# Kernel optimization log

Hardware: AMD Instinct MI355X
Metric: run time of the kernel (lower is better)

Reference implementation:

```python
import jax, jax.numpy as jnp
import numpy as np


def bilinear_align_corners(p, H, W):
    # p: [B, C, h, w] -> [B, C, H, W], matches F.interpolate(mode='bilinear', align_corners=True)
    b, c, h, w = p.shape
    ys = jnp.linspace(0.0, h - 1.0, H)
    xs = jnp.linspace(0.0, w - 1.0, W)
    y0 = jnp.floor(ys).astype(jnp.int32)
    x0 = jnp.floor(xs).astype(jnp.int32)
    y1 = jnp.minimum(y0 + 1, h - 1)
    x1 = jnp.minimum(x0 + 1, w - 1)
    wy = (ys - y0.astype(p.dtype))[:, None]          # [H,1]
    wx = (xs - x0.astype(p.dtype))                   # [W]
    rows = p[:, :, y0, :] * (1 - wy) + p[:, :, y1, :] * wy   # [B,C,H,w]
    out = rows[:, :, :, x0] * (1 - wx) + rows[:, :, :, x1] * wx  # [B,C,H,W]
    return out


def conv1x1(x, W, b):
    return jnp.einsum('bchw,oc->bohw', x, W) + b[None, :, None, None]


def scan_axis(feat, A_bar, B_bar, axis):
    # selective recurrence h_i = A_i * stop_grad(h_{i-1}) + B_i * x_i along `axis`
    f = jnp.moveaxis(feat, axis, 0)
    A = jnp.moveaxis(A_bar, axis, 0)
    B = jnp.moveaxis(B_bar, axis, 0)

    def step(prev, inp):
        a_i, b_i, x_i = inp
        h = a_i * jax.lax.stop_gradient(prev) + b_i * x_i
        return h, h

    _, hs = jax.lax.scan(step, jnp.zeros_like(f[0]), (A, B, f))
    return jnp.moveaxis(hs, 0, axis)


def setup_inputs() -> dict:
    key = jax.random.key(0)
    ks = jax.random.split(key, 12)
    Bsz, Cin, H, W = 4, 64, 256, 256
    hid = 128
    s_in = 1.0 / np.sqrt(Cin)
    s_hid = 1.0 / np.sqrt(hid)
    return {
        'x': jax.random.normal(ks[0], (Bsz, Cin, H, W), jnp.float32),
        'prior': jax.random.normal(ks[1], (Bsz, 1, 64, 64), jnp.float32),
        'W_in': jax.random.uniform(ks[2], (hid, Cin), jnp.float32, -s_in, s_in),
        'b_in': jax.random.uniform(ks[3], (hid,), jnp.float32, -s_in, s_in),
        'W_out': jax.random.uniform(ks[4], (Cin, hid), jnp.float32, -s_hid, s_hid),
        'b_out': jax.random.uniform(ks[5], (Cin,), jnp.float32, -s_hid, s_hid),
        'W_delta': jax.random.uniform(ks[6], (hid, hid), jnp.float32, -s_hid, s_hid),
        'b_delta': jax.random.uniform(ks[7], (hid,), jnp.float32, -s_hid, s_hid),
        'W_B': jax.random.uniform(ks[8], (hid, hid), jnp.float32, -s_hid, s_hid),
        'b_B': jax.random.uniform(ks[9], (hid,), jnp.float32, -s_hid, s_hid),
        'A_param': jax.random.normal(ks[10], (hid,), jnp.float32),
        'lambda_delta': jnp.float32(0.1),
        'alpha': jnp.float32(0.1),
        'gamma': jnp.float32(0.1),
    }


def reference(x, prior, W_in, b_in, W_out, b_out, W_delta, b_delta, W_B, b_B,
              A_param, lambda_delta, alpha, gamma):
    Bsz, C, H, W = x.shape
    prior_up = jnp.clip(bilinear_align_corners(prior, H, W), -1.0, 1.0)
    x_proj = conv1x1(x, W_in, b_in)
    delta = jax.nn.softplus(conv1x1(x_proj, W_delta, b_delta) + lambda_delta * prior_up)
    B_k = conv1x1(x_proj, W_B, b_B) * (1.0 + alpha * prior_up)
    A = -jnp.exp(A_param)[None, :, None, None]
    A_bar = jnp.exp(delta * A)
    B_bar = delta * B_k
    # dim=0 in torch code scans along W (axis 3); dim=1 scans along H (axis 2)
    scanned = scan_axis(x_proj, A_bar, B_bar, 3) + scan_axis(x_proj, A_bar, B_bar, 2)
    out = conv1x1(scanned, W_out, b_out)
    return (x + gamma * out, prior_up)
```

## Files before the change

kernel.cpp:

```cpp
#include <hip/hip_runtime.h>
#include <hip/hip_bf16.h>

#define OUT1 16777216
#define BIG  33554432

typedef _Float16 half8 __attribute__((ext_vector_type(8)));
typedef float    floatx4 __attribute__((ext_vector_type(4)));

struct __align__(8) h4s { _Float16 x, y, z, w; };
__device__ inline void store4h(_Float16* p, float4 v){
    h4s t; t.x = (_Float16)v.x; t.y = (_Float16)v.y; t.z = (_Float16)v.z; t.w = (_Float16)v.w;
    *(h4s*)p = t;
}

__global__ __launch_bounds__(256) void k_prior(const float* __restrict__ prior, float* __restrict__ pu){
    int i = blockIdx.x*256 + threadIdx.x;
    int b = i >> 16;
    int rem = i & 65535;
    int yy = rem >> 8, xx = rem & 255;
    const float scale = 63.0f/255.0f;
    float sy = yy*scale, sx = xx*scale;
    int y0 = min((int)floorf(sy), 63), x0 = min((int)floorf(sx), 63);
    int y1 = min(y0+1, 63), x1 = min(x0+1, 63);
    float wy = sy - (float)y0, wx = sx - (float)x0;
    const float* pb = prior + (b<<12);
    float v00 = pb[(y0<<6)+x0], v01 = pb[(y0<<6)+x1];
    float v10 = pb[(y1<<6)+x0], v11 = pb[(y1<<6)+x1];
    float r0 = v00*(1.f-wy) + v10*wy;
    float r1 = v01*(1.f-wy) + v11*wy;
    float v  = r0*(1.f-wx) + r1*wx;
    pu[i] = fminf(fmaxf(v, -1.f), 1.f);
}

__global__ __launch_bounds__(256) void k_comb(const float* __restrict__ W_in, const float* __restrict__ b_in,
        const float* __restrict__ W_delta, const float* __restrict__ b_delta,
        const float* __restrict__ W_B, const float* __restrict__ b_B,
        const float* __restrict__ A_param, const float* __restrict__ W_out,
        _Float16* __restrict__ Wch, float* __restrict__ bcv, float* __restrict__ negA,
        _Float16* __restrict__ Wof){
    int i = blockIdx.x*256 + threadIdx.x;
    if (i < 24576){
        int r = i >> 6, c = i & 63;
        float v;
        if (r < 128) v = W_in[i];
        else if (r < 256){
            int rr = r-128; float s = 0.f;
            for (int k=0;k<128;k++) s = fmaf(W_delta[(rr<<7)+k], W_in[(k<<6)+c], s);
            v = s;
        } else {
            int rr = r-256; float s = 0.f;
            for (int k=0;k<128;k++) s = fmaf(W_B[(rr<<7)+k], W_in[(k<<6)+c], s);
            v = s;
        }
        Wch[i] = (_Float16)v;
    } else if (i < 24960){
        int r = i - 24576; float v;
        if (r < 128) v = b_in[r];
        else if (r < 256){
            int rr=r-128; float s = b_delta[rr];
            for (int k=0;k<128;k++) s = fmaf(W_delta[(rr<<7)+k], b_in[k], s);
            v = s;
        } else {
            int rr=r-256; float s = b_B[rr];
            for (int k=0;k<128;k++) s = fmaf(W_B[(rr<<7)+k], b_in[k], s);
            v = s;
        }
        bcv[r] = v;
    } else if (i < 25088){
        negA[i-24960] = -expf(A_param[i-24960]);
    } else if (i < 33280){
        Wof[i-25088] = (_Float16)W_out[i-25088];
    }
}

__global__ __launch_bounds__(512, 4) void k_proj_mfma(const float* __restrict__ x, const float* __restrict__ pu,
        const _Float16* __restrict__ Wch, const float* __restrict__ bcv, const float* __restrict__ negA,
        const float* __restrict__ lam_p, const float* __restrict__ alp_p,
        _Float16* __restrict__ Ab, _Float16* __restrict__ Uu){
    __shared__ _Float16 Ws[24576];

    const int t    = threadIdx.x;
    const int lane = t & 63;
    const int wave = t >> 6;
    const int col  = lane & 15;
    const int quad = lane >> 4;

    const int blk = blockIdx.x;
    const int b   = blk >> 9;
    const int p0  = (blk & 511) << 7;
    const int pxw = p0 + (wave << 4);

    {
        const float4* wsrc = (const float4*)Wch;
        #pragma unroll
        for (int i = 0; i < 6; i++){
            int c = t + (i << 9);
            int row = c >> 3, part = c & 7;
            float4 v = wsrc[c];
            int byteoff = ((row << 7) + (part << 4)) ^ ((row & 7) << 4);
            *(float4*)((char*)Ws + byteoff) = v;
        }
    }

    const float* xb = x + ((size_t)b<<22) + pxw + col;
    half8 aX0, aX1;
    #pragma unroll
    for (int j = 0; j < 8; j++){
        aX0[j] = (_Float16)xb[(size_t)(quad*8 + j) << 16];
        aX1[j] = (_Float16)xb[(size_t)(quad*8 + j + 32) << 16];
    }

    const float lamv = lam_p[0], alpv = alp_p[0];
    float4 puv4 = *(const float4*)(pu + (b<<16) + pxw + (quad<<2));
    float lpu[4], apu[4];
    #pragma unroll
    for (int r = 0; r < 4; r++){
        float pv = ((const float*)&puv4)[r];
        lpu[r] = lamv * pv;
        apu[r] = fmaf(alpv, pv, 1.f);
    }

    __syncthreads();

    const int qb = quad << 4;

    #pragma unroll 1
    for (int ct = 0; ct < 8; ct++){
        int rI = (ct << 4) + col;
        int xr = (rI & 7) << 4;
        int bI = ((rI << 7) + qb) ^ xr;
        half8 wI0 = *(const half8*)((char*)Ws + bI);
        half8 wI1 = *(const half8*)((char*)Ws + (bI ^ 64) + (64 & ~(bI & 0)) - ((bI & 64) ? 64 : -0));
        wI1 = *(const half8*)((char*)Ws + ((((rI << 7) + 64 + qb)) ^ xr));
        half8 wD0 = *(const half8*)((char*)Ws + ((((rI + 128) << 7) + qb) ^ xr));
        half8 wD1 = *(const half8*)((char*)Ws + ((((rI + 128) << 7) + 64 + qb) ^ xr));
        half8 wB0 = *(const half8*)((char*)Ws + ((((rI + 256) << 7) + qb) ^ xr));
        half8 wB1 = *(const half8*)((char*)Ws + ((((rI + 256) << 7) + 64 + qb) ^ xr));

        floatx4 aI = (floatx4){0.f,0.f,0.f,0.f};
        floatx4 aD = (floatx4){0.f,0.f,0.f,0.f};
        floatx4 aB = (floatx4){0.f,0.f,0.f,0.f};
        aI = __builtin_amdgcn_mfma_f32_16x16x32_f16(aX0, wI0, aI, 0, 0, 0);
        aD = __builtin_amdgcn_mfma_f32_16x16x32_f16(aX0, wD0, aD, 0, 0, 0);
        aB = __builtin_amdgcn_mfma_f32_16x16x32_f16(aX0, wB0, aB, 0, 0, 0);
        aI = __builtin_amdgcn_mfma_f32_16x16x32_f16(aX1, wI1, aI, 0, 0, 0);
        aD = __builtin_amdgcn_mfma_f32_16x16x32_f16(aX1, wD1, aD, 0, 0, 0);
        aB = __builtin_amdgcn_mfma_f32_16x16x32_f16(aX1, wB1, aB, 0, 0, 0);

        int c = (ct<<4) + col;
        float biasI = bcv[c], biasD = bcv[128+c], biasB = bcv[256+c], nA = negA[c];
        h4s oa, ou;
        #pragma unroll
        for (int r = 0; r < 4; r++){
            float sI = aI[r] + biasI;
            float sD = aD[r] + biasD;
            float sB = aB[r] + biasB;
            float dpre  = sD + lpu[r];
            float delta = fmaxf(dpre, 0.f) + __logf(1.f + __expf(-fabsf(dpre)));
            float ab    = __expf(nA * delta);
            float uu    = delta * sB * apu[r] * sI;
            (&oa.x)[r] = (_Float16)ab;
            (&ou.x)[r] = (_Float16)uu;
        }
        size_t o = ((size_t)((b<<7) + c)<<16) + pxw + (quad<<2);
        *(h4s*)(Ab+o) = oa;
        *(h4s*)(Uu+o) = ou;
    }
}

__global__ __launch_bounds__(256) void k_scan_w(const _Float16* __restrict__ Ab, const _Float16* __restrict__ Uu,
                                                _Float16* __restrict__ Sw){
    int r    = (blockIdx.x<<2) + (threadIdx.x>>6);
    int lane = threadIdx.x & 63;
    size_t base = ((size_t)r<<8) + (lane<<2);
    h4s a4 = *(const h4s*)(Ab+base);
    h4s u4 = *(const h4s*)(Uu+base);
    float ax=(float)a4.x, ay=(float)a4.y, az=(float)a4.z, aw=(float)a4.w;
    float ux=(float)u4.x, uy=(float)u4.y, uz=(float)u4.z, uw=(float)u4.w;
    float A = ax, U = ux;
    U = fmaf(ay, U, uy); A *= ay;
    U = fmaf(az, U, uz); A *= az;
    U = fmaf(aw, U, uw); A *= aw;
    #pragma unroll
    for (int off=1; off<64; off<<=1){
        float Apv = __shfl_up(A, off, 64);
        float Upv = __shfl_up(U, off, 64);
        if (lane >= off){ U = fmaf(A, Upv, U); A *= Apv; }
    }
    float h = __shfl_up(U, 1, 64);
    if (lane == 0) h = 0.f;
    float4 o;
    h = fmaf(ax, h, ux); o.x = h;
    h = fmaf(ay, h, uy); o.y = h;
    h = fmaf(az, h, uz); o.z = h;
    h = fmaf(aw, h, uw); o.w = h;
    store4h(Sw+base, o);
}

__global__ __launch_bounds__(256) void k_scan_h(const _Float16* __restrict__ AbH, const _Float16* __restrict__ UuH,
                                                const _Float16* __restrict__ Sw, _Float16* __restrict__ Sh){
    int t   = blockIdx.x*256 + threadIdx.x;
    int col = t >> 8;
    int w   = t & 255;
    size_t base = ((size_t)col<<16) + w;
    float h = 0.f;
    #pragma unroll 4
    for (int hh=0; hh<256; hh++){
        size_t idx = base + ((size_t)hh<<8);
        float a = (float)AbH[idx];
        float u = (float)UuH[idx];
        float s = (float)Sw[idx];
        h = fmaf(a, h, u);
        Sh[idx] = (_Float16)(h + s);
    }
}

__global__ __launch_bounds__(256, 4) void k_out_mfma(const float* __restrict__ x, const _Float16* __restrict__ Sh,
        const _Float16* __restrict__ Wof, const float* __restrict__ bout, const float* __restrict__ gam_p,
        float* __restrict__ out){
    const int t    = threadIdx.x;
    const int lane = t & 63;
    const int wave = t >> 6;
    const int col  = lane & 15;
    const int quad = lane >> 4;
    const int b    = blockIdx.x >> 8;
    const int p0   = (blockIdx.x & 255) << 8;
    const int wn0  = wave << 6;

    const _Float16* shb = Sh + ((size_t)b<<23) + p0 + wn0;

    floatx4 acc[4][4];
    #pragma unroll
    for (int mt = 0; mt < 4; mt++)
        #pragma unroll
        for (int nt = 0; nt < 4; nt++)
            acc[mt][nt] = (floatx4){0.f,0.f,0.f,0.f};

    #pragma unroll
    for (int kc = 0; kc < 4; kc++){
        half8 af[4];
        #pragma unroll
        for (int mt = 0; mt < 4; mt++)
            #pragma unroll
            for (int j = 0; j < 8; j++)
                af[mt][j] = shb[((size_t)(kc*32 + quad*8 + j)<<16) + mt*16 + col];
        half8 bf[4];
        #pragma unroll
        for (int nt = 0; nt < 4; nt++)
            bf[nt] = *(const half8*)(Wof + (nt*16 + col)*128 + kc*32 + quad*8);
        #pragma unroll
        for (int mt = 0; mt < 4; mt++)
            #pragma unroll
            for (int nt = 0; nt < 4; nt++)
                acc[mt][nt] = __builtin_amdgcn_mfma_f32_16x16x32_f16(af[mt], bf[nt], acc[mt][nt], 0, 0, 0);
    }

    const float gv = gam_p[0];
    #pragma unroll
    for (int nt = 0; nt < 4; nt++){
        int o = nt*16 + col;
        float bo = bout[o];
        #pragma unroll
        for (int mt = 0; mt < 4; mt++){
            size_t idx = (((size_t)(b*64 + o))<<16) + p0 + wn0 + mt*16 + (quad<<2);
            float4 xv = *(const float4*)(x + idx);
            float4 ov;
            ov.x = fmaf(gv, acc[mt][nt][0] + bo, xv.x);
            ov.y = fmaf(gv, acc[mt][nt][1] + bo, xv.y);
            ov.z = fmaf(gv, acc[mt][nt][2] + bo, xv.z);
            ov.w = fmaf(gv, acc[mt][nt][3] + bo, xv.w);
            *(float4*)(out + idx) = ov;
        }
    }
}

extern "C" void kernel_launch(void* const* d_in, const int* in_sizes, int n_in,
                              void* d_out, int out_size, void* d_ws, size_t ws_size,
                              hipStream_t stream){
    const float* x       = (const float*)d_in[0];
    const float* prior   = (const float*)d_in[1];
    const float* W_in    = (const float*)d_in[2];
    const float* b_in    = (const float*)d_in[3];
    const float* W_out   = (const float*)d_in[4];
    const float* b_out   = (const float*)d_in[5];
    const float* W_delta = (const float*)d_in[6];
    const float* b_delta = (const float*)d_in[7];
    const float* W_B     = (const float*)d_in[8];
    const float* b_B     = (const float*)d_in[9];
    const float* A_param = (const float*)d_in[10];
    const float* lam     = (const float*)d_in[11];
    const float* alp     = (const float*)d_in[12];
    const float* gam     = (const float*)d_in[13];

    float* out = (float*)d_out;
    float* pu  = out + OUT1;

    float* ws        = (float*)d_ws;
    _Float16* Wch    = (_Float16*)ws;
    float* bcv       = ws + 12288;
    float* negA      = ws + 12672;
    _Float16* Wof    = (_Float16*)(ws + 12800);
    _Float16* AbH    = (_Float16*)(ws + 32768);
    _Float16* UuH    = AbH + BIG;
    _Float16* Sh     = UuH + BIG;
    _Float16* Sw     = (_Float16*)out;

    hipLaunchKernelGGL(k_prior,  dim3(1024),  dim3(256), 0, stream, prior, pu);
    hipLaunchKernelGGL(k_comb,   dim3(130),   dim3(256), 0, stream, W_in, b_in, W_delta, b_delta,
                       W_B, b_B, A_param, W_out, Wch, bcv, negA, Wof);
    hipLaunchKernelGGL(k_proj_mfma, dim3(2048), dim3(512), 0, stream,
                       x, pu, Wch, bcv, negA, lam, alp, AbH, UuH);
    hipLaunchKernelGGL(k_scan_w, dim3(32768), dim3(256), 0, stream, AbH, UuH, Sw);
    hipLaunchKernelGGL(k_scan_h, dim3(512),   dim3(256), 0, stream, AbH, UuH, Sw, Sh);
    hipLaunchKernelGGL(k_out_mfma, dim3(1024), dim3(256), 0, stream, x, Sh, Wof, b_out, gam, out);
}
```

Before: 326.0 us.

## Make projection kernel persistent over four pixel chunks with prefetched x loads

The projection kernel now handles four 128-pixel chunks per block (512 blocks instead of 2048). This amortizes the shared-memory weight staging across chunks and software-prefetches the next chunk's x values into registers while the current chunk's MFMAs run. Bias, delta bias, B bias and -exp(A) are packed into one float4 table so each channel needs a single vector load. The cost is more registers per thread, which may lower occupancy, and fewer blocks to spread across CUs.

```diff
diff --git a/kernel.cpp b/kernel.cpp
--- a/kernel.cpp
+++ b/kernel.cpp
@@ -37,7 +37,7 @@
         const float* __restrict__ W_B, const float* __restrict__ b_B,
         const float* __restrict__ A_param, const float* __restrict__ W_out,
         _Float16* __restrict__ Wch, float* __restrict__ bcv, float* __restrict__ negA,
-        _Float16* __restrict__ Wof){
+        _Float16* __restrict__ Wof, float* __restrict__ bct){
     int i = blockIdx.x*256 + threadIdx.x;
     if (i < 24576){
         int r = i >> 6, c = i & 63;
@@ -70,11 +70,28 @@
         negA[i-24960] = -expf(A_param[i-24960]);
     } else if (i < 33280){
         Wof[i-25088] = (_Float16)W_out[i-25088];
+    } else if (i < 33792){
+        int j = i - 33280;
+        int c = j >> 2, comp = j & 3;
+        float v;
+        if (comp == 0) v = b_in[c];
+        else if (comp == 1){
+            float s = b_delta[c];
+            for (int k=0;k<128;k++) s = fmaf(W_delta[(c<<7)+k], b_in[k], s);
+            v = s;
+        } else if (comp == 2){
+            float s = b_B[c];
+            for (int k=0;k<128;k++) s = fmaf(W_B[(c<<7)+k], b_in[k], s);
+            v = s;
+        } else {
+            v = -expf(A_param[c]);
+        }
+        bct[j] = v;
     }
 }
 
 __global__ __launch_bounds__(512, 4) void k_proj_mfma(const float* __restrict__ x, const float* __restrict__ pu,
-        const _Float16* __restrict__ Wch, const float* __restrict__ bcv, const float* __restrict__ negA,
+        const _Float16* __restrict__ Wch, const float* __restrict__ bct,
         const float* __restrict__ lam_p, const float* __restrict__ alp_p,
         _Float16* __restrict__ Ab, _Float16* __restrict__ Uu){
     __shared__ _Float16 Ws[24576];
@@ -85,10 +102,9 @@
     const int col  = lane & 15;
     const int quad = lane >> 4;
 
-    const int blk = blockIdx.x;
-    const int b   = blk >> 9;
-    const int p0  = (blk & 511) << 7;
-    const int pxw = p0 + (wave << 4);
+    const int bl      = blockIdx.x;
+    const int b       = bl >> 7;
+    const int px_base = (bl & 127) << 9;
 
     {
         const float4* wsrc = (const float4*)Wch;
@@ -102,69 +118,93 @@
         }
     }
 
-    const float* xb = x + ((size_t)b<<22) + pxw + col;
-    half8 aX0, aX1;
-    #pragma unroll
-    for (int j = 0; j < 8; j++){
-        aX0[j] = (_Float16)xb[(size_t)(quad*8 + j) << 16];
-        aX1[j] = (_Float16)xb[(size_t)(quad*8 + j + 32) << 16];
-    }
-
     const float lamv = lam_p[0], alpv = alp_p[0];
-    float4 puv4 = *(const float4*)(pu + (b<<16) + pxw + (quad<<2));
-    float lpu[4], apu[4];
-    #pragma unroll
-    for (int r = 0; r < 4; r++){
-        float pv = ((const float*)&puv4)[r];
-        lpu[r] = lamv * pv;
-        apu[r] = fmaf(alpv, pv, 1.f);
+    const float* xcol = x + ((size_t)b<<22) + col;
+
+    float xf0[8], xf1[8];
+    {
+        const float* xp = xcol + px_base + (wave<<4);
+        #pragma unroll
+        for (int j = 0; j < 8; j++){
+            xf0[j] = xp[(size_t)(quad*8 + j) << 16];
+            xf1[j] = xp[(size_t)(quad*8 + j + 32) << 16];
+        }
     }
 
     __syncthreads();
 
     const int qb = quad << 4;
+    const char* wsb = (const char*)Ws;
 
     #pragma unroll 1
-    for (int ct = 0; ct < 8; ct++){
-        int rI = (ct << 4) + col;
-        int xr = (rI & 7) << 4;
-        int bI = ((rI << 7) + qb) ^ xr;
-        half8 wI0 = *(const half8*)((char*)Ws + bI);
-        half8 wI1 = *(const half8*)((char*)Ws + (bI ^ 64) + (64 & ~(bI & 0)) - ((bI & 64) ? 64 : -0));
-        wI1 = *(const half8*)((char*)Ws + ((((rI << 7) + 64 + qb)) ^ xr));
-        half8 wD0 = *(const half8*)((char*)Ws + ((((rI + 128) << 7) + qb) ^ xr));
-        half8 wD1 = *(const half8*)((char*)Ws + ((((rI + 128) << 7) + 64 + qb) ^ xr));
-        half8 wB0 = *(const half8*)((char*)Ws + ((((rI + 256) << 7) + qb) ^ xr));
-        half8 wB1 = *(const half8*)((char*)Ws + ((((rI + 256) << 7) + 64 + qb) ^ xr));
-
-        floatx4 aI = (floatx4){0.f,0.f,0.f,0.f};
-        floatx4 aD = (floatx4){0.f,0.f,0.f,0.f};
-        floatx4 aB = (floatx4){0.f,0.f,0.f,0.f};
-        aI = __builtin_amdgcn_mfma_f32_16x16x32_f16(aX0, wI0, aI, 0, 0, 0);
-        aD = __builtin_amdgcn_mfma_f32_16x16x32_f16(aX0, wD0, aD, 0, 0, 0);
-        aB = __builtin_amdgcn_mfma_f32_16x16x32_f16(aX0, wB0, aB, 0, 0, 0);
-        aI = __builtin_amdgcn_mfma_f32_16x16x32_f16(aX1, wI1, aI, 0, 0, 0);
-        aD = __builtin_amdgcn_mfma_f32_16x16x32_f16(aX1, wD1, aD, 0, 0, 0);
-        aB = __builtin_amdgcn_mfma_f32_16x16x32_f16(aX1, wB1, aB, 0, 0, 0);
-
-        int c = (ct<<4) + col;
-        float biasI = bcv[c], biasD = bcv[128+c], biasB = bcv[256+c], nA = negA[c];
-        h4s oa, ou;
+    for (int ch = 0; ch < 4; ch++){
+        const int pxw = px_base + (ch << 7) + (wave << 4);
+
+        half8 aX0, aX1;
+        #pragma unroll
+        for (int j = 0; j < 8; j++){
+            aX0[j] = (_Float16)xf0[j];
+            aX1[j] = (_Float16)xf1[j];
+        }
+
+        if (ch < 3){
+            const float* xn = xcol + pxw + 128;
+            #pragma unroll
+            for (int j = 0; j < 8; j++){
+                xf0[j] = xn[(size_t)(quad*8 + j) << 16];
+                xf1[j] = xn[(size_t)(quad*8 + j + 32) << 16];
+            }
+        }
+
+        float4 puv4 = *(const float4*)(pu + (b<<16) + pxw + (quad<<2));
+        float lpu[4], apu[4];
         #pragma unroll
         for (int r = 0; r < 4; r++){
-            float sI = aI[r] + biasI;
-            float sD = aD[r] + biasD;
-            float sB = aB[r] + biasB;
-            float dpre  = sD + lpu[r];
-            float delta = fmaxf(dpre, 0.f) + __logf(1.f + __expf(-fabsf(dpre)));
-            float ab    = __expf(nA * delta);
-            float uu    = delta * sB * apu[r] * sI;
-            (&oa.x)[r] = (_Float16)ab;
-            (&ou.x)[r] = (_Float16)uu;
-        }
-        size_t o = ((size_t)((b<<7) + c)<<16) + pxw + (quad<<2);
-        *(h4s*)(Ab+o) = oa;
-        *(h4s*)(Uu+o) = ou;
+            float pv = ((const float*)&puv4)[r];
+            lpu[r] = lamv * pv;
+            apu[r] = fmaf(alpv, pv, 1.f);
+        }
+
+        #pragma unroll 2
+        for (int ct = 0; ct < 8; ct++){
+            int rI = (ct << 4) + col;
+            int xr = (rI & 7) << 4;
+            half8 wI0 = *(const half8*)(wsb + ((( rI       << 7) +      qb) ^ xr));
+            half8 wI1 = *(const half8*)(wsb + ((( rI       << 7) + 64 + qb) ^ xr));
+            half8 wD0 = *(const half8*)(wsb + ((((rI + 128)<< 7) +      qb) ^ xr));
+            half8 wD1 = *(const half8*)(wsb + ((((rI + 128)<< 7) + 64 + qb) ^ xr));
+            half8 wB0 = *(const half8*)(wsb + ((((rI + 256)<< 7) +      qb) ^ xr));
+            half8 wB1 = *(const half8*)(wsb + ((((rI + 256)<< 7) + 64 + qb) ^ xr));
+
+            floatx4 aI = (floatx4){0.f,0.f,0.f,0.f};
+            floatx4 aD = (floatx4){0.f,0.f,0.f,0.f};
+            floatx4 aB = (floatx4){0.f,0.f,0.f,0.f};
+            aI = __builtin_amdgcn_mfma_f32_16x16x32_f16(aX0, wI0, aI, 0, 0, 0);
+            aD = __builtin_amdgcn_mfma_f32_16x16x32_f16(aX0, wD0, aD, 0, 0, 0);
+            aB = __builtin_amdgcn_mfma_f32_16x16x32_f16(aX0, wB0, aB, 0, 0, 0);
+            aI = __builtin_amdgcn_mfma_f32_16x16x32_f16(aX1, wI1, aI, 0, 0, 0);
+            aD = __builtin_amdgcn_mfma_f32_16x16x32_f16(aX1, wD1, aD, 0, 0, 0);
+            aB = __builtin_amdgcn_mfma_f32_16x16x32_f16(aX1, wB1, aB, 0, 0, 0);
+
+            int c = (ct<<4) + col;
+            float4 bv = *(const float4*)(bct + (c<<2));
+            h4s oa, ou;
+            #pragma unroll
+            for (int r = 0; r < 4; r++){
+                float sI = aI[r] + bv.x;
+                float sD = aD[r] + bv.y;
+                float sB = aB[r] + bv.z;
+                float dpre  = sD + lpu[r];
+                float delta = fmaxf(dpre, 0.f) + __logf(1.f + __expf(-fabsf(dpre)));
+                float ab    = __expf(bv.w * delta);
+                float uu    = delta * sB * apu[r] * sI;
+                (&oa.x)[r] = (_Float16)ab;
+                (&ou.x)[r] = (_Float16)uu;
+            }
+            size_t o = ((size_t)((b<<7) + c)<<16) + pxw + (quad<<2);
+            *(h4s*)(Ab+o) = oa;
+            *(h4s*)(Uu+o) = ou;
+        }
     }
 }
 
@@ -300,16 +340,17 @@
     float* bcv       = ws + 12288;
     float* negA      = ws + 12672;
     _Float16* Wof    = (_Float16*)(ws + 12800);
+    float* bct       = ws + 16896;
     _Float16* AbH    = (_Float16*)(ws + 32768);
     _Float16* UuH    = AbH + BIG;
     _Float16* Sh     = UuH + BIG;
     _Float16* Sw     = (_Float16*)out;
 
     hipLaunchKernelGGL(k_prior,  dim3(1024),  dim3(256), 0, stream, prior, pu);
-    hipLaunchKernelGGL(k_comb,   dim3(130),   dim3(256), 0, stream, W_in, b_in, W_delta, b_delta,
-                       W_B, b_B, A_param, W_out, Wch, bcv, negA, Wof);
-    hipLaunchKernelGGL(k_proj_mfma, dim3(2048), dim3(512), 0, stream,
-                       x, pu, Wch, bcv, negA, lam, alp, AbH, UuH);
+    hipLaunchKernelGGL(k_comb,   dim3(132),   dim3(256), 0, stream, W_in, b_in, W_delta, b_delta,
+                       W_B, b_B, A_param, W_out, Wch, bcv, negA, Wof, bct);
+    hipLaunchKernelGGL(k_proj_mfma, dim3(512), dim3(512), 0, stream,
+                       x, pu, Wch, bct, lam, alp, AbH, UuH);
     hipLaunchKernelGGL(k_scan_w, dim3(32768), dim3(256), 0, stream, AbH, UuH, Sw);
     hipLaunchKernelGGL(k_scan_h, dim3(512),   dim3(256), 0, stream, AbH, UuH, Sw, Sh);
     hipLaunchKernelGGL(k_out_mfma, dim3(1024), dim3(256), 0, stream, x, Sh, Wof, b_out, gam, out);
```

Result: no change. 331.2 us (+1.6%).
